# Performance work log

Hardware: AMD Instinct MI355X
Metric: run time of the kernel (lower is better)

## Reference

```python
import jax, jax.numpy as jnp
import numpy as np

N = 50000
E = 800000
IN = 128
HEADS = 4
C = 32  # out_features per head
HC = HEADS * C


def setup_inputs() -> dict:
    key = jax.random.key(0)
    ks = jax.random.split(key, 10)
    s_in = 1.0 / np.sqrt(IN)
    x = jax.random.normal(ks[0], (N, IN), dtype=jnp.float32)
    edge_index = jax.random.randint(ks[1], (2, E), 0, N, dtype=jnp.int64)
    Wq = jax.random.normal(ks[2], (IN, HC), dtype=jnp.float32) * s_in
    bq = jnp.zeros((HC,), dtype=jnp.float32)
    Wk = jax.random.normal(ks[3], (IN, HC), dtype=jnp.float32) * s_in
    bk = jnp.zeros((HC,), dtype=jnp.float32)
    Wv = jax.random.normal(ks[4], (IN, HC), dtype=jnp.float32) * s_in
    bv = jnp.zeros((HC,), dtype=jnp.float32)
    Wskip = jax.random.normal(ks[5], (IN, HC), dtype=jnp.float32) * s_in
    bskip = jnp.zeros((HC,), dtype=jnp.float32)
    return {"x": x, "edge_index": edge_index, "Wq": Wq, "bq": bq,
            "Wk": Wk, "bk": bk, "Wv": Wv, "bv": bv,
            "Wskip": Wskip, "bskip": bskip}


def reference(x, edge_index, Wq, bq, Wk, bk, Wv, bv, Wskip, bskip):
    src = edge_index[0]  # message source j
    dst = edge_index[1]  # message target i

    q = (x @ Wq + bq).reshape(N, HEADS, C)
    k = (x @ Wk + bk).reshape(N, HEADS, C)
    v = (x @ Wv + bv).reshape(N, HEADS, C)

    # per-edge attention logits: [E, H]
    logits = jnp.einsum('ehc,ehc->eh', q[dst], k[src]) / jnp.sqrt(
        jnp.asarray(C, dtype=x.dtype))

    # segment softmax over incoming edges of each target node
    seg_max = jax.ops.segment_max(logits, dst, num_segments=N)
    seg_max = jnp.where(jnp.isfinite(seg_max), seg_max, 0.0)
    expd = jnp.exp(logits - seg_max[dst])
    seg_sum = jax.ops.segment_sum(expd, dst, num_segments=N)
    alpha = expd / (seg_sum[dst] + 1e-16)  # [E, H]

    # scatter-add weighted values: [N, H, C]
    msgs = alpha[:, :, None] * v[src]
    out = jax.ops.segment_sum(msgs, dst, num_segments=N)
    out = out.reshape(N, HC) + (x @ Wskip + bskip)  # root/skip connection

    # LeakyReLU(negative_slope=0.2)
    return jnp.where(out >= 0, out, 0.2 * out)
```

## Files before the change

### kernel.cpp

```cpp
#include <hip/hip_runtime.h>

#define N_NODES 50000
#define E_EDGES 800000
#define IN_F 128
#define HC 128
#define ROWTILES 3125
#define GEMM_BLOCKS 781
#define HIST_BLOCKS 1563
#define CAP 64

typedef __attribute__((ext_vector_type(8))) short short8;
typedef __attribute__((ext_vector_type(4))) float floatx4;

__device__ __forceinline__ unsigned short f2bf(float f) {
    union { float f; unsigned u; } x; x.f = f;
    unsigned r = x.u + 0x7FFF + ((x.u >> 16) & 1);
    return (unsigned short)(r >> 16);
}
__device__ __forceinline__ float bflo(unsigned u) {
    union { unsigned u; float f; } c; c.u = u << 16; return c.f;
}
__device__ __forceinline__ float bfhi(unsigned u) {
    union { unsigned u; float f; } c; c.u = u & 0xFFFF0000u; return c.f;
}
__device__ __forceinline__ int swz16(int b) { return b ^ (((b >> 9)  & 3) << 5); }
__device__ __forceinline__ int swz32(int b) { return b ^ (((b >> 10) & 3) << 5); }

__global__ __launch_bounds__(512) void hist_k(
    const int* __restrict__ src, const int* __restrict__ dst,
    int* __restrict__ cnt, int* __restrict__ ssrc)
{
    int e = blockIdx.x * 512 + threadIdx.x;
    if (e < E_EDGES) {
        int d = dst[e];
        int r = atomicAdd(&cnt[d], 1);
        if (r < CAP) ssrc[(size_t)d * CAP + r] = src[e];
    }
}

__global__ __launch_bounds__(512) void gemm_k(
    const float* __restrict__ x,
    const float* __restrict__ Wq, const float* __restrict__ Wk,
    const float* __restrict__ Wv, const float* __restrict__ Ws,
    const float* __restrict__ bq, const float* __restrict__ bk,
    const float* __restrict__ bv, const float* __restrict__ bs,
    unsigned short* __restrict__ q, unsigned short* __restrict__ k,
    unsigned short* __restrict__ v, float* __restrict__ out)
{
    __shared__ __align__(16) unsigned char lds[6 * 2048 + 2 * 4096];

    const int tid = threadIdx.x;
    const int wv = tid >> 6;
    const int lane = tid & 63;
    const int cg = wv >> 1, hf = wv & 1;
    const int l16 = lane & 15, kh = lane >> 4;

    const float* Wsec = cg == 0 ? Wq : cg == 1 ? Wk : cg == 2 ? Wv : Ws;
    const float* bsec = cg == 0 ? bq : cg == 1 ? bk : cg == 2 ? bv : bs;

    short8 breg[4][4];
    float bias_[4];
#pragma unroll
    for (int n = 0; n < 4; n++) {
        const int col = (hf * 4 + n) * 16 + l16;
        bias_[n] = bsec[col];
#pragma unroll
        for (int ks = 0; ks < 4; ks++) {
            short8 bb;
#pragma unroll
            for (int j = 0; j < 8; j++)
                bb[j] = (short)f2bf(Wsec[(size_t)(ks * 32 + kh * 8 + j) * HC + col]);
            breg[n][ks] = bb;
        }
    }

    unsigned char* Eb = lds + wv * 2048;
    unsigned char* Ef = lds + 12288 + hf * 4096;
    unsigned short* dstb = (cg == 0) ? q : (cg == 1) ? k : v;

    for (int rt = blockIdx.x; rt < ROWTILES; rt += GEMM_BLOCKS) {
        const size_t row = (size_t)rt * 16 + l16;

        short8 a[4];
#pragma unroll
        for (int ks = 0; ks < 4; ks++) {
            const float* p0 = x + row * IN_F + ks * 32 + kh * 8;
            float4 lo = *(const float4*)p0;
            float4 hi = *(const float4*)(p0 + 4);
            short8 aa;
            aa[0] = (short)f2bf(lo.x); aa[1] = (short)f2bf(lo.y);
            aa[2] = (short)f2bf(lo.z); aa[3] = (short)f2bf(lo.w);
            aa[4] = (short)f2bf(hi.x); aa[5] = (short)f2bf(hi.y);
            aa[6] = (short)f2bf(hi.z); aa[7] = (short)f2bf(hi.w);
            a[ks] = aa;
        }

        floatx4 acc[4];
#pragma unroll
        for (int n = 0; n < 4; n++) acc[n] = {0.f, 0.f, 0.f, 0.f};
#pragma unroll
        for (int ks = 0; ks < 4; ks++)
#pragma unroll
            for (int n = 0; n < 4; n++)
                acc[n] = __builtin_amdgcn_mfma_f32_16x16x32_bf16(a[ks], breg[n][ks], acc[n], 0, 0, 0);

        if (cg < 3) {
#pragma unroll
            for (int n = 0; n < 4; n++) {
#pragma unroll
                for (int r = 0; r < 4; r++) {
                    int boff = ((kh * 4 + r) * 64 + n * 16 + l16) * 2;
                    *(unsigned short*)(Eb + swz16(boff)) = f2bf(acc[n][r] + bias_[n]);
                }
            }
            unsigned short* gout = dstb + (size_t)rt * 16 * HC + hf * 64;
#pragma unroll
            for (int i = 0; i < 2; i++) {
                int idx = i * 64 + lane;
                uint4 val = *(const uint4*)(Eb + swz16(idx * 16));
                int r = idx >> 3, cb = (idx & 7) * 8;
                *(uint4*)(gout + r * HC + cb) = val;
            }
        } else {
#pragma unroll
            for (int n = 0; n < 4; n++) {
#pragma unroll
                for (int r = 0; r < 4; r++) {
                    int boff = ((kh * 4 + r) * 64 + n * 16 + l16) * 4;
                    *(float*)(Ef + swz32(boff)) = acc[n][r] + bias_[n];
                }
            }
            float* gout = out + (size_t)rt * 16 * HC + hf * 64;
#pragma unroll
            for (int i = 0; i < 4; i++) {
                int idx = i * 64 + lane;
                float4 val = *(const float4*)(Ef + swz32(idx * 16));
                int r = idx >> 4, cb = (idx & 15) * 4;
                *(float4*)(gout + r * HC + cb) = val;
            }
        }
    }
}

__global__ __launch_bounds__(256) void node_attn(
    const unsigned short* __restrict__ q, const unsigned short* __restrict__ k,
    const unsigned short* __restrict__ v, const int* __restrict__ cnt,
    const int* __restrict__ ssrc, float* __restrict__ out)
{
    const int wave = (blockIdx.x * 256 + threadIdx.x) >> 6;
    if (wave >= N_NODES) return;
    const int lane = threadIdx.x & 63;
    const int node = wave;

    union { unsigned u; float f; } cv;
    const unsigned uq = *(const unsigned*)(q + (size_t)node * HC + lane * 2);
    cv.u = uq << 16;          float qx = cv.f;
    cv.u = uq & 0xFFFF0000u;  float qy = cv.f;

    float accx = 0.f, accy = 0.f, ssum = 0.f;
    int deg = __builtin_amdgcn_readfirstlane(cnt[node]);
    if (deg > CAP) deg = CAP;
    const int* sp = ssrc + (size_t)node * CAP;
    const float scale = 0.17677669529663687f;

    int e = 0;
    for (; e + 3 < deg; e += 4) {
        const int j0 = sp[e],     j1 = sp[e + 1];
        const int j2 = sp[e + 2], j3 = sp[e + 3];
        const unsigned uk0 = *(const unsigned*)(k + (size_t)j0 * HC + lane * 2);
        const unsigned uk1 = *(const unsigned*)(k + (size_t)j1 * HC + lane * 2);
        const unsigned uk2 = *(const unsigned*)(k + (size_t)j2 * HC + lane * 2);
        const unsigned uk3 = *(const unsigned*)(k + (size_t)j3 * HC + lane * 2);
        const unsigned uv0 = *(const unsigned*)(v + (size_t)j0 * HC + lane * 2);
        const unsigned uv1 = *(const unsigned*)(v + (size_t)j1 * HC + lane * 2);
        const unsigned uv2 = *(const unsigned*)(v + (size_t)j2 * HC + lane * 2);
        const unsigned uv3 = *(const unsigned*)(v + (size_t)j3 * HC + lane * 2);
        float p0, p1, p2, p3;
        { float kx, ky;
          cv.u = uk0 << 16; kx = cv.f; cv.u = uk0 & 0xFFFF0000u; ky = cv.f;
          p0 = qx * kx + qy * ky;
          cv.u = uk1 << 16; kx = cv.f; cv.u = uk1 & 0xFFFF0000u; ky = cv.f;
          p1 = qx * kx + qy * ky;
          cv.u = uk2 << 16; kx = cv.f; cv.u = uk2 & 0xFFFF0000u; ky = cv.f;
          p2 = qx * kx + qy * ky;
          cv.u = uk3 << 16; kx = cv.f; cv.u = uk3 & 0xFFFF0000u; ky = cv.f;
          p3 = qx * kx + qy * ky; }
#pragma unroll
        for (int off = 1; off <= 8; off <<= 1) {
            p0 += __shfl_xor(p0, off);
            p1 += __shfl_xor(p1, off);
            p2 += __shfl_xor(p2, off);
            p3 += __shfl_xor(p3, off);
        }
        const float w0 = __expf(p0 * scale);
        const float w1 = __expf(p1 * scale);
        const float w2 = __expf(p2 * scale);
        const float w3 = __expf(p3 * scale);
        { float vx, vy;
          cv.u = uv0 << 16; vx = cv.f; cv.u = uv0 & 0xFFFF0000u; vy = cv.f;
          accx += w0 * vx; accy += w0 * vy;
          cv.u = uv1 << 16; vx = cv.f; cv.u = uv1 & 0xFFFF0000u; vy = cv.f;
          accx += w1 * vx; accy += w1 * vy;
          cv.u = uv2 << 16; vx = cv.f; cv.u = uv2 & 0xFFFF0000u; vy = cv.f;
          accx += w2 * vx; accy += w2 * vy;
          cv.u = uv3 << 16; vx = cv.f; cv.u = uv3 & 0xFFFF0000u; vy = cv.f;
          accx += w3 * vx; accy += w3 * vy; }
        ssum += (w0 + w1) + (w2 + w3);
    }
    for (; e < deg; e++) {
        const int j0 = sp[e];
        const unsigned uk0 = *(const unsigned*)(k + (size_t)j0 * HC + lane * 2);
        const unsigned uv0 = *(const unsigned*)(v + (size_t)j0 * HC + lane * 2);
        float kx, ky;
        cv.u = uk0 << 16; kx = cv.f; cv.u = uk0 & 0xFFFF0000u; ky = cv.f;
        float p0 = qx * kx + qy * ky;
        p0 += __shfl_xor(p0, 1);
        p0 += __shfl_xor(p0, 2);
        p0 += __shfl_xor(p0, 4);
        p0 += __shfl_xor(p0, 8);
        const float w0 = __expf(p0 * scale);
        float vx, vy;
        cv.u = uv0 << 16; vx = cv.f; cv.u = uv0 & 0xFFFF0000u; vy = cv.f;
        accx += w0 * vx; accy += w0 * vy;
        ssum += w0;
    }

    const float inv = 1.0f / (ssum + 1e-16f);
    const float2 sk = *(const float2*)(out + (size_t)node * HC + lane * 2);
    float ox = accx * inv + sk.x;
    float oy = accy * inv + sk.y;
    ox = ox >= 0.f ? ox : 0.2f * ox;
    oy = oy >= 0.f ? oy : 0.2f * oy;
    *(float2*)(out + (size_t)node * HC + lane * 2) = make_float2(ox, oy);
}

extern "C" void kernel_launch(void* const* d_in, const int* in_sizes, int n_in,
                              void* d_out, int out_size, void* d_ws, size_t ws_size,
                              hipStream_t stream)
{
    const float* x    = (const float*)d_in[0];
    const int*   ei   = (const int*)d_in[1];
    const float* Wq   = (const float*)d_in[2];
    const float* bq   = (const float*)d_in[3];
    const float* Wk   = (const float*)d_in[4];
    const float* bk   = (const float*)d_in[5];
    const float* Wv   = (const float*)d_in[6];
    const float* bv   = (const float*)d_in[7];
    const float* Wsk  = (const float*)d_in[8];
    const float* bsk  = (const float*)d_in[9];
    float* out = (float*)d_out;

    char* w = (char*)d_ws;
    const size_t NFB = (size_t)N_NODES * HC * sizeof(unsigned short);
    unsigned short* q = (unsigned short*)w;            w += NFB;
    unsigned short* k = (unsigned short*)w;            w += NFB;
    unsigned short* v = (unsigned short*)w;            w += NFB;
    int* cnt  = (int*)w;                               w += N_NODES * sizeof(int);
    int* ssrc = (int*)w;

    const int* srcIdx = ei;
    const int* dstIdx = ei + E_EDGES;

    hipMemsetAsync(cnt, 0, N_NODES * sizeof(int), stream);
    hist_k<<<HIST_BLOCKS, 512, 0, stream>>>(srcIdx, dstIdx, cnt, ssrc);
    gemm_k<<<GEMM_BLOCKS, 512, 0, stream>>>(
        x, Wq, Wk, Wv, Wsk, bq, bk, bv, bsk, q, k, v, out);
    node_attn<<<(N_NODES * 64) / 256, 256, 0, stream>>>(q, k, v, cnt, ssrc, out);
}
```

Baseline: 167.8 us.

## Pre-pack bf16 weights and fuse histogram with GEMM in one launch

```diff
diff --git a/kernel.cpp b/kernel.cpp
--- a/kernel.cpp
+++ b/kernel.cpp
@@ -5,8 +5,8 @@
 #define IN_F 128
 #define HC 128
 #define ROWTILES 3125
-#define GEMM_BLOCKS 781
-#define HIST_BLOCKS 1563
+#define PACK_BLOCKS 32
+#define HIST_BLOCKS 3125
 #define CAP 64
 
 typedef __attribute__((ext_vector_type(8))) short short8;
@@ -23,121 +23,115 @@
 __device__ __forceinline__ float bfhi(unsigned u) {
     union { unsigned u; float f; } c; c.u = u & 0xFFFF0000u; return c.f;
 }
-__device__ __forceinline__ int swz16(int b) { return b ^ (((b >> 9)  & 3) << 5); }
-__device__ __forceinline__ int swz32(int b) { return b ^ (((b >> 10) & 3) << 5); }
-
-__global__ __launch_bounds__(512) void hist_k(
-    const int* __restrict__ src, const int* __restrict__ dst,
-    int* __restrict__ cnt, int* __restrict__ ssrc)
-{
-    int e = blockIdx.x * 512 + threadIdx.x;
-    if (e < E_EDGES) {
-        int d = dst[e];
-        int r = atomicAdd(&cnt[d], 1);
-        if (r < CAP) ssrc[(size_t)d * CAP + r] = src[e];
-    }
-}
-
-__global__ __launch_bounds__(512) void gemm_k(
-    const float* __restrict__ x,
+__device__ __forceinline__ int swzb(int b) { return b ^ (((b >> 10) & 3) << 5); }
+__device__ __forceinline__ int swzf(int b) { return b ^ (((b >> 11) & 3) << 5); }
+
+__global__ __launch_bounds__(256) void pack_w(
     const float* __restrict__ Wq, const float* __restrict__ Wk,
     const float* __restrict__ Wv, const float* __restrict__ Ws,
     const float* __restrict__ bq, const float* __restrict__ bk,
     const float* __restrict__ bv, const float* __restrict__ bs,
+    short* __restrict__ bpack, float* __restrict__ bcat,
+    int* __restrict__ cnt)
+{
+    int t = blockIdx.x * 256 + threadIdx.x;
+    int lane = t & 63, ks = (t >> 6) & 3, nt = t >> 8;
+    int col = nt * 16 + (lane & 15);
+    int sec = col >> 7, c = col & 127;
+    const float* W = sec == 0 ? Wq : sec == 1 ? Wk : sec == 2 ? Wv : Ws;
+    int kbase = ks * 32 + (lane >> 4) * 8;
+    short8 b;
+#pragma unroll
+    for (int j = 0; j < 8; j++) b[j] = (short)f2bf(W[(size_t)(kbase + j) * HC + c]);
+    *(short8*)(bpack + (size_t)t * 8) = b;
+    if (t < 512) {
+        int s2 = t >> 7, c2 = t & 127;
+        bcat[t] = (s2 == 0 ? bq : s2 == 1 ? bk : s2 == 2 ? bv : bs)[c2];
+    }
+    for (int i = t; i < N_NODES; i += PACK_BLOCKS * 256) cnt[i] = 0;
+}
+
+__global__ __launch_bounds__(256) void gemm_hist(
+    const float* __restrict__ x, const short* __restrict__ bpack,
+    const float* __restrict__ bcat,
     unsigned short* __restrict__ q, unsigned short* __restrict__ k,
-    unsigned short* __restrict__ v, float* __restrict__ out)
-{
-    __shared__ __align__(16) unsigned char lds[6 * 2048 + 2 * 4096];
-
-    const int tid = threadIdx.x;
-    const int wv = tid >> 6;
-    const int lane = tid & 63;
-    const int cg = wv >> 1, hf = wv & 1;
+    unsigned short* __restrict__ v, float* __restrict__ out,
+    const int* __restrict__ src, const int* __restrict__ dst,
+    int* __restrict__ cnt, int* __restrict__ ssrc)
+{
+    if (blockIdx.x >= ROWTILES) {
+        int e = (blockIdx.x - ROWTILES) * 256 + threadIdx.x;
+        int d = dst[e];
+        int r = atomicAdd(&cnt[d], 1);
+        if (r < CAP) ssrc[(size_t)d * CAP + r] = src[e];
+        return;
+    }
+    __shared__ __align__(16) unsigned char lds[3 * 4096 + 8192];
+
+    const int rt = blockIdx.x;
+    const int cg = threadIdx.x >> 6;
+    const int lane = threadIdx.x & 63;
     const int l16 = lane & 15, kh = lane >> 4;
 
-    const float* Wsec = cg == 0 ? Wq : cg == 1 ? Wk : cg == 2 ? Wv : Ws;
-    const float* bsec = cg == 0 ? bq : cg == 1 ? bk : cg == 2 ? bv : bs;
-
-    short8 breg[4][4];
-    float bias_[4];
-#pragma unroll
-    for (int n = 0; n < 4; n++) {
-        const int col = (hf * 4 + n) * 16 + l16;
-        bias_[n] = bsec[col];
+    short8 a[4];
+    const size_t row = (size_t)rt * 16 + l16;
+#pragma unroll
+    for (int ks = 0; ks < 4; ks++) {
+        const float* p0 = x + row * IN_F + ks * 32 + kh * 8;
+        float4 lo = *(const float4*)p0;
+        float4 hi = *(const float4*)(p0 + 4);
+        short8 aa;
+        aa[0] = (short)f2bf(lo.x); aa[1] = (short)f2bf(lo.y);
+        aa[2] = (short)f2bf(lo.z); aa[3] = (short)f2bf(lo.w);
+        aa[4] = (short)f2bf(hi.x); aa[5] = (short)f2bf(hi.y);
+        aa[6] = (short)f2bf(hi.z); aa[7] = (short)f2bf(hi.w);
+        a[ks] = aa;
+    }
+
+    unsigned char* Eb = lds + cg * 4096;
+    unsigned char* Ef = lds + 12288;
+
+#pragma unroll
+    for (int nt8 = 0; nt8 < 8; nt8++) {
+        const int nt = cg * 8 + nt8;
+        floatx4 acc = {0.f, 0.f, 0.f, 0.f};
 #pragma unroll
         for (int ks = 0; ks < 4; ks++) {
-            short8 bb;
-#pragma unroll
-            for (int j = 0; j < 8; j++)
-                bb[j] = (short)f2bf(Wsec[(size_t)(ks * 32 + kh * 8 + j) * HC + col]);
-            breg[n][ks] = bb;
-        }
-    }
-
-    unsigned char* Eb = lds + wv * 2048;
-    unsigned char* Ef = lds + 12288 + hf * 4096;
-    unsigned short* dstb = (cg == 0) ? q : (cg == 1) ? k : v;
-
-    for (int rt = blockIdx.x; rt < ROWTILES; rt += GEMM_BLOCKS) {
-        const size_t row = (size_t)rt * 16 + l16;
-
-        short8 a[4];
-#pragma unroll
-        for (int ks = 0; ks < 4; ks++) {
-            const float* p0 = x + row * IN_F + ks * 32 + kh * 8;
-            float4 lo = *(const float4*)p0;
-            float4 hi = *(const float4*)(p0 + 4);
-            short8 aa;
-            aa[0] = (short)f2bf(lo.x); aa[1] = (short)f2bf(lo.y);
-            aa[2] = (short)f2bf(lo.z); aa[3] = (short)f2bf(lo.w);
-            aa[4] = (short)f2bf(hi.x); aa[5] = (short)f2bf(hi.y);
-            aa[6] = (short)f2bf(hi.z); aa[7] = (short)f2bf(hi.w);
-            a[ks] = aa;
-        }
-
-        floatx4 acc[4];
-#pragma unroll
-        for (int n = 0; n < 4; n++) acc[n] = {0.f, 0.f, 0.f, 0.f};
-#pragma unroll
-        for (int ks = 0; ks < 4; ks++)
-#pragma unroll
-            for (int n = 0; n < 4; n++)
-                acc[n] = __builtin_amdgcn_mfma_f32_16x16x32_bf16(a[ks], breg[n][ks], acc[n], 0, 0, 0);
-
+            short8 b = *(const short8*)(bpack + ((size_t)(nt * 4 + ks) * 64 + lane) * 8);
+            acc = __builtin_amdgcn_mfma_f32_16x16x32_bf16(a[ks], b, acc, 0, 0, 0);
+        }
+        const float bias = bcat[cg * 128 + nt8 * 16 + l16];
         if (cg < 3) {
 #pragma unroll
-            for (int n = 0; n < 4; n++) {
-#pragma unroll
-                for (int r = 0; r < 4; r++) {
-                    int boff = ((kh * 4 + r) * 64 + n * 16 + l16) * 2;
-                    *(unsigned short*)(Eb + swz16(boff)) = f2bf(acc[n][r] + bias_[n]);
-                }
-            }
-            unsigned short* gout = dstb + (size_t)rt * 16 * HC + hf * 64;
-#pragma unroll
-            for (int i = 0; i < 2; i++) {
-                int idx = i * 64 + lane;
-                uint4 val = *(const uint4*)(Eb + swz16(idx * 16));
-                int r = idx >> 3, cb = (idx & 7) * 8;
-                *(uint4*)(gout + r * HC + cb) = val;
+            for (int r = 0; r < 4; r++) {
+                int boff = ((kh * 4 + r) * 128 + nt8 * 16 + l16) * 2;
+                *(unsigned short*)(Eb + swzb(boff)) = f2bf(acc[r] + bias);
             }
         } else {
 #pragma unroll
-            for (int n = 0; n < 4; n++) {
-#pragma unroll
-                for (int r = 0; r < 4; r++) {
-                    int boff = ((kh * 4 + r) * 64 + n * 16 + l16) * 4;
-                    *(float*)(Ef + swz32(boff)) = acc[n][r] + bias_[n];
-                }
+            for (int r = 0; r < 4; r++) {
+                int boff = ((kh * 4 + r) * 128 + nt8 * 16 + l16) * 4;
+                *(float*)(Ef + swzf(boff)) = acc[r] + bias;
             }
-            float* gout = out + (size_t)rt * 16 * HC + hf * 64;
-#pragma unroll
-            for (int i = 0; i < 4; i++) {
-                int idx = i * 64 + lane;
-                float4 val = *(const float4*)(Ef + swz32(idx * 16));
-                int r = idx >> 4, cb = (idx & 15) * 4;
-                *(float4*)(gout + r * HC + cb) = val;
-            }
+        }
+    }
+
+    if (cg < 3) {
+        unsigned short* gout = ((cg == 0) ? q : (cg == 1) ? k : v)
+                               + (size_t)rt * 16 * HC;
+#pragma unroll
+        for (int i = 0; i < 4; i++) {
+            int idx = i * 64 + lane;
+            uint4 val = *(const uint4*)(Eb + swzb(idx * 16));
+            *(uint4*)(gout + idx * 8) = val;
+        }
+    } else {
+        float* gout = out + (size_t)rt * 16 * HC;
+#pragma unroll
+        for (int i = 0; i < 8; i++) {
+            int idx = i * 64 + lane;
+            float4 val = *(const float4*)(Ef + swzf(idx * 16));
+            *(float4*)(gout + idx * 4) = val;
         }
     }
 }
@@ -255,15 +249,17 @@
     unsigned short* q = (unsigned short*)w;            w += NFB;
     unsigned short* k = (unsigned short*)w;            w += NFB;
     unsigned short* v = (unsigned short*)w;            w += NFB;
+    short* bpack = (short*)w;                          w += 8192 * 8 * sizeof(short);
+    float* bcat  = (float*)w;                          w += 512 * sizeof(float);
     int* cnt  = (int*)w;                               w += N_NODES * sizeof(int);
     int* ssrc = (int*)w;
 
     const int* srcIdx = ei;
     const int* dstIdx = ei + E_EDGES;
 
-    hipMemsetAsync(cnt, 0, N_NODES * sizeof(int), stream);
-    hist_k<<<HIST_BLOCKS, 512, 0, stream>>>(srcIdx, dstIdx, cnt, ssrc);
-    gemm_k<<<GEMM_BLOCKS, 512, 0, stream>>>(
-        x, Wq, Wk, Wv, Wsk, bq, bk, bv, bsk, q, k, v, out);
+    pack_w<<<PACK_BLOCKS, 256, 0, stream>>>(Wq, Wk, Wv, Wsk, bq, bk, bv, bsk,
+                                            bpack, bcat, cnt);
+    gemm_hist<<<ROWTILES + HIST_BLOCKS, 256, 0, stream>>>(
+        x, bpack, bcat, q, k, v, out, srcIdx, dstIdx, cnt, ssrc);
     node_attn<<<(N_NODES * 64) / 256, 256, 0, stream>>>(q, k, v, cnt, ssrc, out);
 }
```

After: 157.5 us. -6.1%, faster.
